# Kernel optimization log

Hardware: AMD Instinct MI355X
Metric: run time of the kernel (lower is better)

## Reference

```python
import jax, jax.numpy as jnp
import numpy as np

IN_DIM, OUT_DIM = 64, 64
HIDDEN = [64, 64, 64]
D = IN_DIM * OUT_DIM  # number of independent per-edge small MLPs
B = 256


def setup_inputs() -> dict:
    key = jax.random.key(0)
    ks = jax.random.split(key, 10)

    def kaiming(k, shape, fan_in):
        # kaiming_uniform_ with a=0, nonlinearity='relu': bound = sqrt(6/fan_in)
        bound = np.sqrt(6.0 / fan_in)
        return jax.random.uniform(k, shape, jnp.float32, -bound, bound)

    def bias_init(k, shape, fan_in):
        bound = 1.0 / np.sqrt(fan_in)
        return jax.random.uniform(k, shape, jnp.float32, -bound, bound)

    h0, h1, h2 = HIDDEN
    inp = {
        "x": jax.random.normal(ks[0], (B, IN_DIM), jnp.float32),
        # Input_Linear: weight (out_dim, in_dim, h0); fan_in per torch kaiming on this tensor is in_dim*h0,
        # bias uses reset_parameters(1) -> fan_in=1
        "w0": kaiming(ks[1], (OUT_DIM, IN_DIM, h0), IN_DIM * h0),
        "b0": bias_init(ks[2], (D, h0), 1),
        # Linear(d, o=h1, i=h0): weight (d, h1, h0); kaiming fan_in = h0 (last dim), bias fan_in = i = h0
        "w1": kaiming(ks[3], (D, h1, h0), h0),
        "b1": bias_init(ks[4], (D, h1), h0),
        "w2": kaiming(ks[5], (D, h2, h1), h1),
        "b2": bias_init(ks[6], (D, h2), h1),
        # Output_Linear: weight (out_dim, in_dim*h2), fan_in = in_dim*h2
        "wout": kaiming(ks[7], (OUT_DIM, IN_DIM * h2), IN_DIM * h2),
        "bout": bias_init(ks[8], (OUT_DIM,), IN_DIM * h2),
    }
    return inp


def reference(x, w0, b0, w1, b1, w2, b2, wout, bout):
    Bsz = x.shape[0]
    # Input_Linear: broadcast outer product -> (B, out_dim, in_dim, h0) -> (B, d, h0)
    out = x[:, None, :, None] * w0[None, :, :, :]
    out = out.reshape(Bsz, D, HIDDEN[0]) + b0[None, :, :]
    out = jax.nn.relu(out)
    # Hidden per-edge Linear layers: 'doi,Bdi->Bdo'
    out = jnp.einsum('doi,bdi->bdo', w1, out) + b1[None, :, :]
    out = jax.nn.relu(out)
    out = jnp.einsum('doi,bdi->bdo', w2, out) + b2[None, :, :]
    out = jax.nn.relu(out)
    # Output_Linear: (B, d, h2) -> (B, out_dim, in_dim*h2); 'oi,boi->bo'
    xv = out.reshape(Bsz, OUT_DIM, IN_DIM * HIDDEN[-1])
    return jnp.einsum('oi,boi->bo', wout, xv) + bout[None, :]
```

## Files before the change

kernel.cpp:

```cpp
#include <hip/hip_runtime.h>
#include <hip/hip_bf16.h>


#define D_EDGES 4096

typedef __attribute__((ext_vector_type(4))) float f32x4;
typedef __attribute__((ext_vector_type(8))) short bf16x8;

__device__ __forceinline__ unsigned pk2(float a, float b) {
    __hip_bfloat162 h = __float22bfloat162_rn(float2{a, b});
    return *reinterpret_cast<unsigned*>(&h);
}

__device__ __forceinline__ bf16x8 mk8(unsigned a, unsigned b, unsigned c, unsigned d) {
    uint4 u{a, b, c, d};
    return __builtin_bit_cast(bf16x8, u);
}

__device__ __forceinline__ int rho(int n) {
    return (n & 0x23) | ((n & 0x18) >> 1) | ((n & 0x04) << 2);
}

__global__ __launch_bounds__(256, 4) void kan_mfma(
    const float* __restrict__ x,
    const float* __restrict__ w0g,
    const float* __restrict__ b0g,
    const float* __restrict__ w1g,
    const float* __restrict__ b1g,
    const float* __restrict__ w2g,
    const float* __restrict__ b2g,
    const float* __restrict__ woutg,
    float* __restrict__ outbuf,
    int atomic_mode)
{
    const int d = blockIdx.x, o = d >> 6, ii = d & 63;
    const int t = threadIdx.x;
    const int lane = t & 63, wv = t >> 6;

    __shared__ __align__(16) unsigned char W1s[64 * 128];
    __shared__ __align__(16) unsigned char W2s[64 * 128];
    __shared__ __align__(16) float sx[256];
    __shared__ __align__(16) float sw0[64], sb0[64], sb1[64], sb2[64], swo[64];

    {
        const int orow = t >> 2, q = t & 3;
        const int prow = rho(orow);
        const unsigned swz1  = (unsigned)((prow & 7) << 4);
        const unsigned base1 = (unsigned)(prow * 128);
        const unsigned swz2  = (unsigned)((orow & 7) << 4);
        const unsigned base2 = (unsigned)(orow * 128);
        const float* s1 = w1g + (size_t)d * 4096 + orow * 64 + q * 16;
        const float* s2 = w2g + (size_t)d * 4096 + orow * 64 + q * 16;

        float4 a0 = ((const float4*)s1)[0], a1 = ((const float4*)s1)[1];
        float4 a2 = ((const float4*)s1)[2], a3 = ((const float4*)s1)[3];
        uint4 u0 = { pk2(a0.x, a0.y), pk2(a0.z, a0.w), pk2(a1.x, a1.y), pk2(a1.z, a1.w) };
        uint4 u1 = { pk2(a2.x, a2.y), pk2(a2.z, a2.w), pk2(a3.x, a3.y), pk2(a3.z, a3.w) };
        *(uint4*)&W1s[base1 + ((unsigned)(q * 32)      ^ swz1)] = u0;
        *(uint4*)&W1s[base1 + ((unsigned)(q * 32 + 16) ^ swz1)] = u1;

        a0 = ((const float4*)s2)[0]; a1 = ((const float4*)s2)[1];
        a2 = ((const float4*)s2)[2]; a3 = ((const float4*)s2)[3];
        uint4 v0 = { pk2(a0.x, a0.y), pk2(a0.z, a0.w), pk2(a1.x, a1.y), pk2(a1.z, a1.w) };
        uint4 v1 = { pk2(a2.x, a2.y), pk2(a2.z, a2.w), pk2(a3.x, a3.y), pk2(a3.z, a3.w) };
        *(uint4*)&W2s[base2 + ((unsigned)(q * 32)      ^ swz2)] = v0;
        *(uint4*)&W2s[base2 + ((unsigned)(q * 32 + 16) ^ swz2)] = v1;
    }
    sx[t] = x[t * 64 + ii];
    if (t < 64) {
        sw0[t] = w0g[(size_t)d * 64 + t];
        sb0[t] = b0g[(size_t)d * 64 + t];
        sb1[t] = b1g[(size_t)d * 64 + t];
        sb2[t] = b2g[(size_t)d * 64 + t];
        swo[t] = woutg[(size_t)o * 4096 + ii * 64 + t];
    }
    __syncthreads();

    const int arow = lane & 15;
    const int kb   = (lane >> 4) * 16;
    const int g8   = (lane >> 4) * 8;
    const unsigned lswz = (unsigned)((lane & 7) << 4);
    const int r0 = (lane >> 4) * 4;
    const f32x4 zero4 = { 0.f, 0.f, 0.f, 0.f };

    bf16x8 wf1[4][2];
#pragma unroll
    for (int nt = 0; nt < 4; ++nt)
#pragma unroll
        for (int ks = 0; ks < 2; ++ks)
            wf1[nt][ks] = *(const bf16x8*)&W1s[(nt * 16 + arow) * 128 +
                            ((unsigned)(ks * 64 + kb) ^ lswz)];

    bf16x8 wf2[4][2];

#pragma unroll
    for (int mti = 0; mti < 4; ++mti) {
        const float xm = sx[wv * 64 + mti * 16 + arow];

        f32x4 a1[4] = { zero4, zero4, zero4, zero4 };
#pragma unroll
        for (int ks = 0; ks < 2; ++ks) {
            const int k0 = ks * 32 + g8;
            float4 wa = *(const float4*)&sw0[k0];
            float4 wb = *(const float4*)&sw0[k0 + 4];
            float4 ba = *(const float4*)&sb0[k0];
            float4 bb = *(const float4*)&sb0[k0 + 4];
            float v0 = fmaxf(fmaf(xm, wa.x, ba.x), 0.f);
            float v1 = fmaxf(fmaf(xm, wa.y, ba.y), 0.f);
            float v2 = fmaxf(fmaf(xm, wa.z, ba.z), 0.f);
            float v3 = fmaxf(fmaf(xm, wa.w, ba.w), 0.f);
            float v4 = fmaxf(fmaf(xm, wb.x, bb.x), 0.f);
            float v5 = fmaxf(fmaf(xm, wb.y, bb.y), 0.f);
            float v6 = fmaxf(fmaf(xm, wb.z, bb.z), 0.f);
            float v7 = fmaxf(fmaf(xm, wb.w, bb.w), 0.f);
            bf16x8 bh = mk8(pk2(v0, v1), pk2(v2, v3), pk2(v4, v5), pk2(v6, v7));
#pragma unroll
            for (int nt = 0; nt < 4; ++nt)
                a1[nt] = __builtin_amdgcn_mfma_f32_16x16x32_bf16(
                    wf1[nt][ks], bh, a1[nt], 0, 0, 0);
        }

        if (mti == 0) {
#pragma unroll
            for (int nt = 0; nt < 4; ++nt)
#pragma unroll
                for (int ks = 0; ks < 2; ++ks)
                    wf2[nt][ks] = *(const bf16x8*)&W2s[(nt * 16 + arow) * 128 +
                                    ((unsigned)(ks * 64 + kb) ^ lswz)];
        }

        unsigned l0, h0, l1, h1, l2, h2, l3, h3;
#define PACK_NT(nt, LO, HI)                                                     \
        {                                                                       \
            const int bb_ = (((nt) >> 1) << 5) + (((nt) & 1) << 2) + g8;        \
            float4 bv = *(const float4*)&sb1[bb_];                              \
            LO = pk2(fmaxf(a1[nt][0] + bv.x, 0.f), fmaxf(a1[nt][1] + bv.y, 0.f)); \
            HI = pk2(fmaxf(a1[nt][2] + bv.z, 0.f), fmaxf(a1[nt][3] + bv.w, 0.f)); \
        }
        PACK_NT(0, l0, h0)
        PACK_NT(1, l1, h1)
        PACK_NT(2, l2, h2)
        PACK_NT(3, l3, h3)
#undef PACK_NT
        bf16x8 f0 = mk8(l0, h0, l1, h1);
        bf16x8 f1 = mk8(l2, h2, l3, h3);

        f32x4 a2[4] = { zero4, zero4, zero4, zero4 };
#pragma unroll
        for (int nt = 0; nt < 4; ++nt) {
            a2[nt] = __builtin_amdgcn_mfma_f32_16x16x32_bf16(
                wf2[nt][0], f0, a2[nt], 0, 0, 0);
            a2[nt] = __builtin_amdgcn_mfma_f32_16x16x32_bf16(
                wf2[nt][1], f1, a2[nt], 0, 0, 0);
        }

        float p = 0.f;
#pragma unroll
        for (int nt = 0; nt < 4; ++nt) {
            float4 bv = *(const float4*)&sb2[nt * 16 + r0];
            float4 wo = *(const float4*)&swo[nt * 16 + r0];
            p = fmaf(fmaxf(a2[nt][0] + bv.x, 0.f), wo.x, p);
            p = fmaf(fmaxf(a2[nt][1] + bv.y, 0.f), wo.y, p);
            p = fmaf(fmaxf(a2[nt][2] + bv.z, 0.f), wo.z, p);
            p = fmaf(fmaxf(a2[nt][3] + bv.w, 0.f), wo.w, p);
        }
        p += __shfl_xor(p, 16);
        p += __shfl_xor(p, 32);
        const int b = wv * 64 + mti * 16 + arow;
        if (lane < 16) {
            if (atomic_mode) atomicAdd(&outbuf[b * 64 + o], p);
            else             outbuf[(size_t)d * 256 + b] = p;
        }
    }
}

__global__ __launch_bounds__(64) void kan_reduce(
    const float* __restrict__ partial,
    const float* __restrict__ bout,
    float* __restrict__ y)
{
    const int o  = blockIdx.x;
    const int b  = blockIdx.y * 64 + threadIdx.x;
    float acc = bout[o];
    const float* p = partial + (size_t)o * (64 * 256) + b;
#pragma unroll
    for (int i = 0; i < 64; ++i)
        acc += p[i * 256];
    y[b * 64 + o] = acc;
}

__global__ __launch_bounds__(256) void kan_init_out(const float* __restrict__ bout,
                                                    float* __restrict__ y)
{
    const int idx = blockIdx.x * 256 + threadIdx.x;
    y[idx] = bout[idx & 63];
}

extern "C" void kernel_launch(void* const* d_in, const int* in_sizes, int n_in,
                              void* d_out, int out_size, void* d_ws, size_t ws_size,
                              hipStream_t stream) {
    const float* x    = (const float*)d_in[0];
    const float* w0   = (const float*)d_in[1];
    const float* b0   = (const float*)d_in[2];
    const float* w1   = (const float*)d_in[3];
    const float* b1   = (const float*)d_in[4];
    const float* w2   = (const float*)d_in[5];
    const float* b2   = (const float*)d_in[6];
    const float* wout = (const float*)d_in[7];
    const float* bout = (const float*)d_in[8];
    float* y = (float*)d_out;

    const size_t partial_bytes = (size_t)D_EDGES * 256 * sizeof(float);

    if (ws_size >= partial_bytes) {
        float* partial = (float*)d_ws;
        kan_mfma<<<D_EDGES, 256, 0, stream>>>(x, w0, b0, w1, b1, w2, b2, wout, partial, 0);
        kan_reduce<<<dim3(64, 4), 64, 0, stream>>>(partial, bout, y);
    } else {
        kan_init_out<<<64, 256, 0, stream>>>(bout, y);
        kan_mfma<<<D_EDGES, 256, 0, stream>>>(x, w0, b0, w1, b1, w2, b2, wout, y, 1);
    }
}
```

Measured before the change: 40.67 us.

## Load MFMA weight fragments directly from global memory, bypassing LDS staging

Drops the shared-memory staging of W1/W2 (convert to bf16, swizzled LDS store, barrier, LDS read). Each wave now loads its fragments straight from global memory with float4 reads and converts them in registers. W1 is loaded before the barrier and W2 inside the first iteration, so global latency can overlap other work. This removes 16 KB of LDS per block, which may raise occupancy. The cost is that all four waves load the same weights (four times the global/L2 traffic), and the per-lane access pattern is less coalesced.

Result: slower. 75.92 us (+86.7%).

```diff
diff --git a/kernel.cpp b/kernel.cpp
--- a/kernel.cpp
+++ b/kernel.cpp
@@ -17,8 +17,14 @@
     return __builtin_bit_cast(bf16x8, u);
 }
 
-__device__ __forceinline__ int rho(int n) {
-    return (n & 0x23) | ((n & 0x18) >> 1) | ((n & 0x04) << 2);
+__device__ __forceinline__ bf16x8 ldfrag(const float* __restrict__ p) {
+    float4 a = ((const float4*)p)[0];
+    float4 b = ((const float4*)p)[1];
+    return mk8(pk2(a.x, a.y), pk2(a.z, a.w), pk2(b.x, b.y), pk2(b.z, b.w));
+}
+
+__device__ __forceinline__ int rho_inv(int p) {
+    return (p & 0x23) | ((p & 0x0C) << 1) | ((p & 0x10) >> 2);
 }
 
 __global__ __launch_bounds__(256, 4) void kan_mfma(
@@ -37,35 +43,9 @@
     const int t = threadIdx.x;
     const int lane = t & 63, wv = t >> 6;
 
-    __shared__ __align__(16) unsigned char W1s[64 * 128];
-    __shared__ __align__(16) unsigned char W2s[64 * 128];
     __shared__ __align__(16) float sx[256];
     __shared__ __align__(16) float sw0[64], sb0[64], sb1[64], sb2[64], swo[64];
 
-    {
-        const int orow = t >> 2, q = t & 3;
-        const int prow = rho(orow);
-        const unsigned swz1  = (unsigned)((prow & 7) << 4);
-        const unsigned base1 = (unsigned)(prow * 128);
-        const unsigned swz2  = (unsigned)((orow & 7) << 4);
-        const unsigned base2 = (unsigned)(orow * 128);
-        const float* s1 = w1g + (size_t)d * 4096 + orow * 64 + q * 16;
-        const float* s2 = w2g + (size_t)d * 4096 + orow * 64 + q * 16;
-
-        float4 a0 = ((const float4*)s1)[0], a1 = ((const float4*)s1)[1];
-        float4 a2 = ((const float4*)s1)[2], a3 = ((const float4*)s1)[3];
-        uint4 u0 = { pk2(a0.x, a0.y), pk2(a0.z, a0.w), pk2(a1.x, a1.y), pk2(a1.z, a1.w) };
-        uint4 u1 = { pk2(a2.x, a2.y), pk2(a2.z, a2.w), pk2(a3.x, a3.y), pk2(a3.z, a3.w) };
-        *(uint4*)&W1s[base1 + ((unsigned)(q * 32)      ^ swz1)] = u0;
-        *(uint4*)&W1s[base1 + ((unsigned)(q * 32 + 16) ^ swz1)] = u1;
-
-        a0 = ((const float4*)s2)[0]; a1 = ((const float4*)s2)[1];
-        a2 = ((const float4*)s2)[2]; a3 = ((const float4*)s2)[3];
-        uint4 v0 = { pk2(a0.x, a0.y), pk2(a0.z, a0.w), pk2(a1.x, a1.y), pk2(a1.z, a1.w) };
-        uint4 v1 = { pk2(a2.x, a2.y), pk2(a2.z, a2.w), pk2(a3.x, a3.y), pk2(a3.z, a3.w) };
-        *(uint4*)&W2s[base2 + ((unsigned)(q * 32)      ^ swz2)] = v0;
-        *(uint4*)&W2s[base2 + ((unsigned)(q * 32 + 16) ^ swz2)] = v1;
-    }
     sx[t] = x[t * 64 + ii];
     if (t < 64) {
         sw0[t] = w0g[(size_t)d * 64 + t];
@@ -74,22 +54,24 @@
         sb2[t] = b2g[(size_t)d * 64 + t];
         swo[t] = woutg[(size_t)o * 4096 + ii * 64 + t];
     }
-    __syncthreads();
 
     const int arow = lane & 15;
-    const int kb   = (lane >> 4) * 16;
     const int g8   = (lane >> 4) * 8;
-    const unsigned lswz = (unsigned)((lane & 7) << 4);
     const int r0 = (lane >> 4) * 4;
     const f32x4 zero4 = { 0.f, 0.f, 0.f, 0.f };
 
+    const float* w1base = w1g + (size_t)d * 4096;
+    const float* w2base = w2g + (size_t)d * 4096;
     bf16x8 wf1[4][2];
 #pragma unroll
-    for (int nt = 0; nt < 4; ++nt)
+    for (int nt = 0; nt < 4; ++nt) {
+        const int n1 = rho_inv(nt * 16 + arow);
 #pragma unroll
         for (int ks = 0; ks < 2; ++ks)
-            wf1[nt][ks] = *(const bf16x8*)&W1s[(nt * 16 + arow) * 128 +
-                            ((unsigned)(ks * 64 + kb) ^ lswz)];
+            wf1[nt][ks] = ldfrag(w1base + n1 * 64 + ks * 32 + g8);
+    }
+
+    __syncthreads();
 
     bf16x8 wf2[4][2];
 
@@ -122,11 +104,12 @@
 
         if (mti == 0) {
 #pragma unroll
-            for (int nt = 0; nt < 4; ++nt)
+            for (int nt = 0; nt < 4; ++nt) {
+                const int n2 = nt * 16 + arow;
 #pragma unroll
                 for (int ks = 0; ks < 2; ++ks)
-                    wf2[nt][ks] = *(const bf16x8*)&W2s[(nt * 16 + arow) * 128 +
-                                    ((unsigned)(ks * 64 + kb) ^ lswz)];
+                    wf2[nt][ks] = ldfrag(w2base + n2 * 64 + ks * 32 + g8);
+            }
         }
 
         unsigned l0, h0, l1, h1, l2, h2, l3, h3;
```
